# Kernel tuning notes

Hardware: AMD Instinct MI355X
Metric: run time of the kernel (lower is better)

## Reference

```python
import jax, jax.numpy as jnp
import numpy as np

N, H, F, E, K = 2048, 1024, 4096, 8, 2


def setup_inputs() -> dict:
    key = jax.random.key(0)
    ks = jax.random.split(key, 6)
    x = jax.random.normal(ks[0], (N, H), dtype=jnp.float32)
    mapping = jax.random.randint(ks[1], (N, K), 0, E)
    Wg = jax.random.normal(ks[2], (E, H), dtype=jnp.float32) * (1.0 / np.sqrt(H))
    W1 = jax.random.normal(ks[3], (E, H, F), dtype=jnp.float32) * (1.0 / np.sqrt(H))
    b1 = jnp.zeros((E, F), dtype=jnp.float32)
    W2 = jax.random.normal(ks[4], (E, F, H), dtype=jnp.float32) * (1.0 / np.sqrt(F))
    b2 = jnp.zeros((E, H), dtype=jnp.float32)
    return {"x": x, "mapping": mapping, "Wg": Wg, "W1": W1, "b1": b1, "W2": W2, "b2": b2}


def reference(x, mapping, Wg, W1, b1, W2, b2):
    # Gate logits: note original applies softmax over dim=0 (the token axis).
    logits = jax.nn.softmax(x @ Wg.T, axis=0)  # [N, E]

    # Per-expert MLP. Original sorts tokens by expert, runs per-expert GEMMs on
    # dynamic splits, then unsorts -- mathematically: y[i,k] = MLP_{mapping[i,k]}(x[i]).
    # JIT-friendly dense baseline: run every expert over all tokens, gather per token.
    def mlp(e):
        h = jax.nn.gelu(x @ W1[e] + b1[e])  # [N, F]
        return h @ W2[e] + b2[e]            # [N, H]

    y_all = jnp.stack([mlp(e) for e in range(E)])  # [E, N, H]

    # Gate weights gathered per (token, k), normalized over top-k.
    w = jnp.take_along_axis(logits, mapping, axis=1)  # [N, K]
    w = w / jnp.sum(w, axis=-1, keepdims=True)

    idx = jnp.arange(x.shape[0])
    out = jnp.zeros_like(x)
    for k in range(mapping.shape[1]):
        yk = y_all[mapping[:, k], idx]  # [N, H] gather per token's k-th expert
        out = out + yk * w[:, k:k + 1]
    return out
```

## Files before the change

### kernel.cpp

```cpp
#include <hip/hip_runtime.h>

#define N_TOK 2048
#define HD    1024
#define FD    4096
#define NE    8

typedef __attribute__((ext_vector_type(8))) short short8;
typedef __attribute__((ext_vector_type(4))) float floatx4;

__device__ __forceinline__ unsigned short f2bf(float f) {
  unsigned int u = __float_as_uint(f);
  u += 0x7fffu + ((u >> 16) & 1u);
  return (unsigned short)(u >> 16);
}

__device__ __forceinline__ void gl2lds16(const unsigned short* g, unsigned short* l) {
  __builtin_amdgcn_global_load_lds(
      (const __attribute__((address_space(1))) unsigned int*)g,
      (__attribute__((address_space(3))) unsigned int*)l, 16, 0, 0);
}

__device__ __forceinline__ float gelu_tanh(float x) {
  float t = 0.7978845608028654f * x * (1.0f + 0.044715f * x * x);
  return 0.5f * x * (1.0f + tanhf(t));
}

__device__ __forceinline__ int poff_of(const int* __restrict__ cnt, int e) {
  int o = 0;
  for (int i = 0; i < e; ++i) o += (cnt[i] + 127) & ~127;
  return o;
}

__global__ void k_gating(const float* __restrict__ x, const float* __restrict__ wg,
                         float* __restrict__ p) {
  int wave = threadIdx.x >> 6;
  int lane = threadIdx.x & 63;
  int n = blockIdx.x * 4 + wave;
  const float4* xr = (const float4*)(x + (size_t)n * HD);
  float4 xv[4];
  #pragma unroll
  for (int i = 0; i < 4; ++i) xv[i] = xr[lane + i * 64];
  for (int e = 0; e < NE; ++e) {
    const float4* wr = (const float4*)(wg + (size_t)e * HD);
    float s = 0.f;
    #pragma unroll
    for (int i = 0; i < 4; ++i) {
      float4 w4 = wr[lane + i * 64];
      s += xv[i].x * w4.x + xv[i].y * w4.y + xv[i].z * w4.z + xv[i].w * w4.w;
    }
    for (int o = 32; o > 0; o >>= 1) s += __shfl_xor(s, o, 64);
    if (lane == 0) p[e * N_TOK + n] = s;
  }
}

__global__ void k_softmax(float* __restrict__ p) {
  int e = blockIdx.x;
  float* col = p + e * N_TOK;
  __shared__ float red[256];
  int t = threadIdx.x;
  float m = -1e30f;
  for (int i = t; i < N_TOK; i += 256) m = fmaxf(m, col[i]);
  red[t] = m; __syncthreads();
  for (int s = 128; s > 0; s >>= 1) { if (t < s) red[t] = fmaxf(red[t], red[t + s]); __syncthreads(); }
  m = red[0]; __syncthreads();
  float sum = 0.f;
  for (int i = t; i < N_TOK; i += 256) { float v = expf(col[i] - m); col[i] = v; sum += v; }
  red[t] = sum; __syncthreads();
  for (int s = 128; s > 0; s >>= 1) { if (t < s) red[t] += red[t + s]; __syncthreads(); }
  float inv = 1.0f / red[0];
  for (int i = t; i < N_TOK; i += 256) col[i] *= inv;
}

__global__ void k_route(const int* __restrict__ mp, const float* __restrict__ p,
                        int* __restrict__ cnt, int* __restrict__ idxl,
                        int* __restrict__ tke, int* __restrict__ tks, float* __restrict__ tkw) {
  int n = blockIdx.x * 256 + threadIdx.x;
  if (n >= N_TOK) return;
  int m0 = mp[n * 2 + 0], m1 = mp[n * 2 + 1];
  if (m0 == m1) {
    int s = atomicAdd(&cnt[m0], 1);
    idxl[m0 * N_TOK + s] = n;
    tke[n * 2] = m0; tks[n * 2] = s; tkw[n * 2] = 1.0f;
    tke[n * 2 + 1] = m0; tks[n * 2 + 1] = s; tkw[n * 2 + 1] = 0.0f;
  } else {
    float p0 = p[m0 * N_TOK + n], p1 = p[m1 * N_TOK + n];
    float inv = 1.0f / (p0 + p1);
    int s0 = atomicAdd(&cnt[m0], 1);
    idxl[m0 * N_TOK + s0] = n;
    tke[n * 2] = m0; tks[n * 2] = s0; tkw[n * 2] = p0 * inv;
    int s1 = atomicAdd(&cnt[m1], 1);
    idxl[m1 * N_TOK + s1] = n;
    tke[n * 2 + 1] = m1; tks[n * 2 + 1] = s1; tkw[n * 2 + 1] = p1 * inv;
  }
}

__global__ void k_gather(const float* __restrict__ x, const int* __restrict__ cnt,
                         const int* __restrict__ idxl, unsigned short* __restrict__ xg) {
  int e = blockIdx.y;
  int r = blockIdx.x;
  int c = cnt[e];
  int pc = (c + 127) & ~127;
  if (r >= pc) return;
  unsigned short* dst = xg + ((size_t)poff_of(cnt, e) + r) * HD;
  int t = threadIdx.x;
  union { unsigned short us[8]; uint4 v; } o;
  if (r < c) {
    const float* src = x + (size_t)idxl[e * N_TOK + r] * HD;
    float4 f0 = ((const float4*)src)[t * 2];
    float4 f1 = ((const float4*)src)[t * 2 + 1];
    o.us[0] = f2bf(f0.x); o.us[1] = f2bf(f0.y); o.us[2] = f2bf(f0.z); o.us[3] = f2bf(f0.w);
    o.us[4] = f2bf(f1.x); o.us[5] = f2bf(f1.y); o.us[6] = f2bf(f1.z); o.us[7] = f2bf(f1.w);
  } else {
    o.v.x = 0u; o.v.y = 0u; o.v.z = 0u; o.v.w = 0u;
  }
  ((uint4*)dst)[t] = o.v;
}

__global__ __launch_bounds__(256) void k_transtile(const float* __restrict__ w1,
                                                   unsigned short* __restrict__ w1t,
                                                   const float* __restrict__ w2,
                                                   unsigned short* __restrict__ w2t) {
  __shared__ float tile[32][129];
  int l = blockIdx.x;
  const float* src; unsigned short* dst; int ncols; size_t tbase;
  int e, nt, kt;
  if (l < 8192) {
    e = l >> 10; nt = (l >> 5) & 31; kt = l & 31;
    src = w1 + (size_t)e * HD * FD; ncols = FD;
    dst = w1t; tbase = (((size_t)e * 32 + nt) * 32 + kt) * 4096;
  } else {
    int l2 = l - 8192;
    e = l2 >> 10; nt = (l2 >> 7) & 7; kt = l2 & 127;
    src = w2 + (size_t)e * FD * HD; ncols = HD;
    dst = w2t; tbase = (((size_t)e * 8 + nt) * 128 + kt) * 4096;
  }
  const int t = threadIdx.x;
  const int c4 = t & 31;
  const int rb = t >> 5;
  #pragma unroll
  for (int i = 0; i < 4; ++i) {
    int r = rb + 8 * i;
    float4 v = *(const float4*)(src + (size_t)(kt * 32 + r) * ncols + nt * 128 + c4 * 4);
    tile[r][c4 * 4 + 0] = v.x; tile[r][c4 * 4 + 1] = v.y;
    tile[r][c4 * 4 + 2] = v.z; tile[r][c4 * 4 + 3] = v.w;
  }
  __syncthreads();
  #pragma unroll
  for (int i = 0; i < 2; ++i) {
    int o = t * 2 + i;
    int n = o >> 2, kc = o & 3;
    union { unsigned short us[8]; uint4 v; } u;
    #pragma unroll
    for (int j = 0; j < 8; ++j) u.us[j] = f2bf(tile[kc * 8 + j][n]);
    *(uint4*)(dst + tbase + (size_t)o * 8) = u.v;
  }
}

__global__ __launch_bounds__(256) void k_gemm1(
    const unsigned short* __restrict__ xg, const unsigned short* __restrict__ w1t,
    const float* __restrict__ b1, const int* __restrict__ cnt,
    unsigned short* __restrict__ h) {
  const int l = blockIdx.x;
  const int r = l & 7;
  const int m = (l >> 3) & 31;
  const int q = l >> 8;
  const int e = q >> 2;
  const int n = ((q & 3) << 3) | r;

  const int c = cnt[e];
  const int mbase = m * 64;
  if (mbase >= c) return;
  const int nbase = n * 128;
  const int po = poff_of(cnt, e);
  const unsigned short* A = xg + ((size_t)po + mbase) * HD;
  const unsigned short* Bt = w1t + (((size_t)e * 32 + n) * 32) * 4096;

  __shared__ unsigned short As[64 * 32];
  __shared__ unsigned short Bs[128 * 32];

  const int tid = threadIdx.x;
  const int wave = tid >> 6, lane = tid & 63;
  const int quad = lane >> 4, lrow = lane & 15;
  const int wn = wave * 32;

  floatx4 acc[4][2];
  #pragma unroll
  for (int i = 0; i < 4; ++i)
    #pragma unroll
    for (int j = 0; j < 2; ++j) acc[i][j] = (floatx4){0.f, 0.f, 0.f, 0.f};

  const int rA = tid >> 2, kA = (tid & 3) * 8;

  for (int kt = 0; kt < HD / 32; ++kt) {
    __syncthreads();
    gl2lds16(A + kt * 32 + (size_t)rA * HD + kA, As + (size_t)wave * 512);
    const unsigned short* gb = Bt + (size_t)kt * 4096 + (size_t)tid * 8;
    gl2lds16(gb,        Bs + (size_t)wave * 512);
    gl2lds16(gb + 2048, Bs + 2048 + (size_t)wave * 512);
    __syncthreads();
    short8 aF[4], bF[2];
    #pragma unroll
    for (int i = 0; i < 4; ++i)
      aF[i] = *(const short8*)(As + (i * 16 + lrow) * 32 + quad * 8);
    #pragma unroll
    for (int j = 0; j < 2; ++j)
      bF[j] = *(const short8*)(Bs + (wn + j * 16 + lrow) * 32 + quad * 8);
    #pragma unroll
    for (int i = 0; i < 4; ++i)
      #pragma unroll
      for (int j = 0; j < 2; ++j)
        acc[i][j] = __builtin_amdgcn_mfma_f32_16x16x32_bf16(aF[i], bF[j], acc[i][j], 0, 0, 0);
  }

  const size_t hrow0 = (size_t)po + mbase;
  #pragma unroll
  for (int i = 0; i < 4; ++i) {
    #pragma unroll
    for (int rr = 0; rr < 4; ++rr) {
      int row = i * 16 + quad * 4 + rr;
      unsigned short* hr = h + (hrow0 + row) * FD + nbase;
      #pragma unroll
      for (int j = 0; j < 2; ++j) {
        int col = wn + j * 16 + lrow;
        float v = acc[i][j][rr] + b1[e * FD + nbase + col];
        hr[col] = f2bf(gelu_tanh(v));
      }
    }
  }
}

__global__ __launch_bounds__(256) void k_gemm2(
    const unsigned short* __restrict__ h, const unsigned short* __restrict__ w2t,
    const int* __restrict__ cnt, unsigned short* __restrict__ ya) {
  const int l = blockIdx.x;
  const int nt = l & 15;
  const int mt = l >> 4;
  const int mbase = mt * 64;
  const int nbase = nt * 64;

  int e = -1, po = 0, ce = 0;
  {
    int o = 0;
    #pragma unroll
    for (int i = 0; i < NE; ++i) {
      int ci = cnt[i];
      int pc = (ci + 127) & ~127;
      if (mbase >= o && mbase < o + pc) { e = i; po = o; ce = ci; }
      o += pc;
    }
  }
  if (e < 0) return;
  if (mbase - po >= ce) return;

  const unsigned short* A = h + (size_t)mbase * FD;
  const unsigned short* Bt = w2t + (((size_t)e * 8 + (nt >> 1)) * 128) * 4096
                                 + (size_t)(nt & 1) * 2048;

  __shared__ unsigned short As[2 * 64 * 32];
  __shared__ unsigned short Bs[2 * 64 * 32];

  const int tid = threadIdx.x;
  const int wave = tid >> 6, lane = tid & 63;
  const int quad = lane >> 4, lrow = lane & 15;
  const int wm = (wave >> 1) * 32, wn = (wave & 1) * 32;

  floatx4 acc[2][2];
  #pragma unroll
  for (int i = 0; i < 2; ++i)
    #pragma unroll
    for (int j = 0; j < 2; ++j) acc[i][j] = (floatx4){0.f, 0.f, 0.f, 0.f};

  const int r0 = tid >> 2, k0 = (tid & 3) * 8;

  for (int kt = 0; kt < FD / 64; ++kt) {
    __syncthreads();
    #pragma unroll
    for (int cc = 0; cc < 2; ++cc) {
      gl2lds16(A + (size_t)r0 * FD + kt * 64 + cc * 32 + k0,
               As + cc * 2048 + (size_t)wave * 512);
      gl2lds16(Bt + (size_t)(kt * 2 + cc) * 4096 + (size_t)tid * 8,
               Bs + cc * 2048 + (size_t)wave * 512);
    }
    __syncthreads();
    #pragma unroll
    for (int cc = 0; cc < 2; ++cc) {
      short8 aF[2], bF[2];
      #pragma unroll
      for (int i = 0; i < 2; ++i)
        aF[i] = *(const short8*)(As + cc * 2048 + (wm + i * 16 + lrow) * 32 + quad * 8);
      #pragma unroll
      for (int j = 0; j < 2; ++j)
        bF[j] = *(const short8*)(Bs + cc * 2048 + (wn + j * 16 + lrow) * 32 + quad * 8);
      #pragma unroll
      for (int i = 0; i < 2; ++i)
        #pragma unroll
        for (int j = 0; j < 2; ++j)
          acc[i][j] = __builtin_amdgcn_mfma_f32_16x16x32_bf16(aF[i], bF[j], acc[i][j], 0, 0, 0);
    }
  }

  #pragma unroll
  for (int i = 0; i < 2; ++i) {
    #pragma unroll
    for (int rr = 0; rr < 4; ++rr) {
      int row = mbase + wm + i * 16 + quad * 4 + rr;
      unsigned short* yr = ya + (size_t)row * HD + nbase;
      #pragma unroll
      for (int j = 0; j < 2; ++j) {
        int col = wn + j * 16 + lrow;
        yr[col] = f2bf(acc[i][j][rr]);
      }
    }
  }
}

__global__ __launch_bounds__(256) void k_combine(
    const unsigned short* __restrict__ ya, const float* __restrict__ b2,
    const int* __restrict__ cnt, const int* __restrict__ tke,
    const int* __restrict__ tks, const float* __restrict__ tkw,
    float* __restrict__ out) {
  int n = blockIdx.x;
  int e0 = tke[n * 2], e1 = tke[n * 2 + 1];
  int p0 = poff_of(cnt, e0) + tks[n * 2];
  int p1 = poff_of(cnt, e1) + tks[n * 2 + 1];
  float w0 = tkw[n * 2], w1 = tkw[n * 2 + 1];
  int c = threadIdx.x * 4;
  union { unsigned short us[4]; ushort2 u2[2]; unsigned long long ll; } y0, y1;
  y0.ll = *(const unsigned long long*)(ya + (size_t)p0 * HD + c);
  y1.ll = *(const unsigned long long*)(ya + (size_t)p1 * HD + c);
  float4 bb0 = *(const float4*)(b2 + (size_t)e0 * HD + c);
  float4 bb1 = *(const float4*)(b2 + (size_t)e1 * HD + c);
  float4 o;
  o.x = w0 * (__uint_as_float((unsigned)y0.us[0] << 16) + bb0.x) + w1 * (__uint_as_float((unsigned)y1.us[0] << 16) + bb1.x);
  o.y = w0 * (__uint_as_float((unsigned)y0.us[1] << 16) + bb0.y) + w1 * (__uint_as_float((unsigned)y1.us[1] << 16) + bb1.y);
  o.z = w0 * (__uint_as_float((unsigned)y0.us[2] << 16) + bb0.z) + w1 * (__uint_as_float((unsigned)y1.us[2] << 16) + bb1.z);
  o.w = w0 * (__uint_as_float((unsigned)y0.us[3] << 16) + bb0.w) + w1 * (__uint_as_float((unsigned)y1.us[3] << 16) + bb1.w);
  *(float4*)(out + (size_t)n * HD + c) = o;
}

extern "C" void kernel_launch(void* const* d_in, const int* in_sizes, int n_in,
                              void* d_out, int out_size, void* d_ws, size_t ws_size,
                              hipStream_t stream) {
  const float* x  = (const float*)d_in[0];
  const int*   mp = (const int*)d_in[1];
  const float* wg = (const float*)d_in[2];
  const float* w1 = (const float*)d_in[3];
  const float* b1 = (const float*)d_in[4];
  const float* w2 = (const float*)d_in[5];
  const float* b2 = (const float*)d_in[6];
  float* out = (float*)d_out;
  char* ws = (char*)d_ws;

  float* p    = (float*)(ws + 0);
  int*   cnt  = (int*)(ws + 65536);
  int*   idxl = (int*)(ws + 66048);
  int*   tke  = (int*)(ws + 131584);
  int*   tks  = (int*)(ws + 147968);
  float* tkw  = (float*)(ws + 164352);
  size_t off = 180736;
  unsigned short* w1t = (unsigned short*)(ws + off);  off += 67108864;
  unsigned short* w2t = (unsigned short*)(ws + off);  off += 67108864;
  unsigned short* xg  = (unsigned short*)(ws + off);  off += 10485760;
  unsigned short* h   = (unsigned short*)(ws + off);  off += 41943040;
  unsigned short* ya  = (unsigned short*)(ws + off);  off += 10485760;

  hipMemsetAsync(cnt, 0, 32, stream);

  k_gating<<<512, 256, 0, stream>>>(x, wg, p);
  k_softmax<<<NE, 256, 0, stream>>>(p);
  k_route<<<NE, 256, 0, stream>>>(mp, p, cnt, idxl, tke, tks, tkw);
  k_transtile<<<16384, 256, 0, stream>>>(w1, w1t, w2, w2t);
  k_gather<<<dim3(N_TOK, NE), 128, 0, stream>>>(x, cnt, idxl, xg);
  k_gemm1<<<8192, 256, 0, stream>>>(xg, w1t, b1, cnt, h);
  k_gemm2<<<80 * 16, 256, 0, stream>>>(h, w2t, cnt, ya);
  k_combine<<<N_TOK, 256, 0, stream>>>(ya, b2, cnt, tke, tks, tkw, out);
}
```

Measured before the change: 488.5 us.

## Fuse fp32 weight conversion and transpose into expert GEMM tile loads

Removes the separate weight transpose/bf16 conversion kernel and its 128MB workspace round trip. Each GEMM block now reads fp32 W1/W2 directly, converts to bf16 in registers, and writes into a XOR-swizzled LDS layout, with half the threads loading weights and half loading activations. Block indices are also remapped so blocks sharing a weight panel run on the same XCD, and gemm2 uses a per-expert grid instead of a scan. The trade-off is that weights are re-read and re-converted by every M tile. Weight loads also become plain fp32 global loads rather than async global-to-LDS copies, which may stall the inner loop.

```diff
diff --git a/kernel.cpp b/kernel.cpp
--- a/kernel.cpp
+++ b/kernel.cpp
@@ -116,64 +116,26 @@
   ((uint4*)dst)[t] = o.v;
 }
 
-__global__ __launch_bounds__(256) void k_transtile(const float* __restrict__ w1,
-                                                   unsigned short* __restrict__ w1t,
-                                                   const float* __restrict__ w2,
-                                                   unsigned short* __restrict__ w2t) {
-  __shared__ float tile[32][129];
-  int l = blockIdx.x;
-  const float* src; unsigned short* dst; int ncols; size_t tbase;
-  int e, nt, kt;
-  if (l < 8192) {
-    e = l >> 10; nt = (l >> 5) & 31; kt = l & 31;
-    src = w1 + (size_t)e * HD * FD; ncols = FD;
-    dst = w1t; tbase = (((size_t)e * 32 + nt) * 32 + kt) * 4096;
-  } else {
-    int l2 = l - 8192;
-    e = l2 >> 10; nt = (l2 >> 7) & 7; kt = l2 & 127;
-    src = w2 + (size_t)e * FD * HD; ncols = HD;
-    dst = w2t; tbase = (((size_t)e * 8 + nt) * 128 + kt) * 4096;
-  }
-  const int t = threadIdx.x;
-  const int c4 = t & 31;
-  const int rb = t >> 5;
-  #pragma unroll
-  for (int i = 0; i < 4; ++i) {
-    int r = rb + 8 * i;
-    float4 v = *(const float4*)(src + (size_t)(kt * 32 + r) * ncols + nt * 128 + c4 * 4);
-    tile[r][c4 * 4 + 0] = v.x; tile[r][c4 * 4 + 1] = v.y;
-    tile[r][c4 * 4 + 2] = v.z; tile[r][c4 * 4 + 3] = v.w;
-  }
-  __syncthreads();
-  #pragma unroll
-  for (int i = 0; i < 2; ++i) {
-    int o = t * 2 + i;
-    int n = o >> 2, kc = o & 3;
-    union { unsigned short us[8]; uint4 v; } u;
-    #pragma unroll
-    for (int j = 0; j < 8; ++j) u.us[j] = f2bf(tile[kc * 8 + j][n]);
-    *(uint4*)(dst + tbase + (size_t)o * 8) = u.v;
-  }
-}
-
 __global__ __launch_bounds__(256) void k_gemm1(
-    const unsigned short* __restrict__ xg, const unsigned short* __restrict__ w1t,
+    const unsigned short* __restrict__ xg, const float* __restrict__ w1,
     const float* __restrict__ b1, const int* __restrict__ cnt,
     unsigned short* __restrict__ h) {
-  const int l = blockIdx.x;
-  const int r = l & 7;
-  const int m = (l >> 3) & 31;
-  const int q = l >> 8;
-  const int e = q >> 2;
-  const int n = ((q & 3) << 3) | r;
+  const int b = blockIdx.x;
+  const int xcd = b & 7;
+  const int idx = b >> 3;
+  const int m = idx & 31;
+  const int panel = ((idx >> 5) << 3) + xcd;
+  const int e  = panel >> 5;
+  const int nt = panel & 31;
 
   const int c = cnt[e];
-  const int mbase = m * 64;
-  if (mbase >= c) return;
-  const int nbase = n * 128;
+  if (m * 64 >= c) return;
   const int po = poff_of(cnt, e);
-  const unsigned short* A = xg + ((size_t)po + mbase) * HD;
-  const unsigned short* Bt = w1t + (((size_t)e * 32 + n) * 32) * 4096;
+  const int nbase = nt * 128;
+  const size_t arow0 = (size_t)po + m * 64;
+
+  const unsigned short* A = xg + arow0 * HD;
+  const float* Bsrc = w1 + (size_t)e * HD * FD + nbase;
 
   __shared__ unsigned short As[64 * 32];
   __shared__ unsigned short Bs[128 * 32];
@@ -189,22 +151,44 @@
     #pragma unroll
     for (int j = 0; j < 2; ++j) acc[i][j] = (floatx4){0.f, 0.f, 0.f, 0.f};
 
-  const int rA = tid >> 2, kA = (tid & 3) * 8;
+  const int bg = tid & 31;
+  const int bq = (tid >> 5) & 3;
 
   for (int kt = 0; kt < HD / 32; ++kt) {
     __syncthreads();
-    gl2lds16(A + kt * 32 + (size_t)rA * HD + kA, As + (size_t)wave * 512);
-    const unsigned short* gb = Bt + (size_t)kt * 4096 + (size_t)tid * 8;
-    gl2lds16(gb,        Bs + (size_t)wave * 512);
-    gl2lds16(gb + 2048, Bs + 2048 + (size_t)wave * 512);
+    if (tid < 128) {
+      float4 f[8];
+      const float* src = Bsrc + (size_t)(kt * 32 + bq * 8) * FD + bg * 4;
+      #pragma unroll
+      for (int j = 0; j < 8; ++j)
+        f[j] = *(const float4*)(src + (size_t)j * FD);
+      #pragma unroll
+      for (int jn = 0; jn < 4; ++jn) {
+        int n = bg * 4 + jn;
+        union { unsigned short us[8]; uint4 v; } u;
+        #pragma unroll
+        for (int j = 0; j < 8; ++j) u.us[j] = f2bf(((const float*)&f[j])[jn]);
+        *(uint4*)(Bs + n * 32 + 8 * (bq ^ (bg & 3))) = u.v;
+      }
+    } else {
+      #pragma unroll
+      for (int i = 0; i < 2; ++i) {
+        int base = ((wave - 2) << 7) + (i << 6);
+        int ch = base + (tid & 63);
+        int row = ch >> 2, ko = (ch & 3) * 8;
+        gl2lds16(A + (size_t)row * HD + kt * 32 + ko, As + (size_t)base * 8);
+      }
+    }
     __syncthreads();
     short8 aF[4], bF[2];
     #pragma unroll
     for (int i = 0; i < 4; ++i)
       aF[i] = *(const short8*)(As + (i * 16 + lrow) * 32 + quad * 8);
     #pragma unroll
-    for (int j = 0; j < 2; ++j)
-      bF[j] = *(const short8*)(Bs + (wn + j * 16 + lrow) * 32 + quad * 8);
+    for (int j = 0; j < 2; ++j) {
+      int n = wn + j * 16 + lrow;
+      bF[j] = *(const short8*)(Bs + n * 32 + 8 * (quad ^ ((n >> 2) & 3)));
+    }
     #pragma unroll
     for (int i = 0; i < 4; ++i)
       #pragma unroll
@@ -212,13 +196,12 @@
         acc[i][j] = __builtin_amdgcn_mfma_f32_16x16x32_bf16(aF[i], bF[j], acc[i][j], 0, 0, 0);
   }
 
-  const size_t hrow0 = (size_t)po + mbase;
   #pragma unroll
   for (int i = 0; i < 4; ++i) {
     #pragma unroll
     for (int rr = 0; rr < 4; ++rr) {
       int row = i * 16 + quad * 4 + rr;
-      unsigned short* hr = h + (hrow0 + row) * FD + nbase;
+      unsigned short* hr = h + (arow0 + row) * FD + nbase;
       #pragma unroll
       for (int j = 0; j < 2; ++j) {
         int col = wn + j * 16 + lrow;
@@ -230,34 +213,27 @@
 }
 
 __global__ __launch_bounds__(256) void k_gemm2(
-    const unsigned short* __restrict__ h, const unsigned short* __restrict__ w2t,
+    const unsigned short* __restrict__ h, const float* __restrict__ w2,
     const int* __restrict__ cnt, unsigned short* __restrict__ ya) {
-  const int l = blockIdx.x;
-  const int nt = l & 15;
-  const int mt = l >> 4;
-  const int mbase = mt * 64;
+  const int b = blockIdx.x;
+  const int xcd = b & 7;
+  const int idx = b >> 3;
+  const int m = idx & 31;
+  const int panel = ((idx >> 5) << 3) + xcd;
+  const int e  = panel >> 4;
+  const int nt = panel & 15;
+
+  const int c = cnt[e];
+  if (m * 64 >= c) return;
+  const int po = poff_of(cnt, e);
   const int nbase = nt * 64;
-
-  int e = -1, po = 0, ce = 0;
-  {
-    int o = 0;
-    #pragma unroll
-    for (int i = 0; i < NE; ++i) {
-      int ci = cnt[i];
-      int pc = (ci + 127) & ~127;
-      if (mbase >= o && mbase < o + pc) { e = i; po = o; ce = ci; }
-      o += pc;
-    }
-  }
-  if (e < 0) return;
-  if (mbase - po >= ce) return;
-
-  const unsigned short* A = h + (size_t)mbase * FD;
-  const unsigned short* Bt = w2t + (((size_t)e * 8 + (nt >> 1)) * 128) * 4096
-                                 + (size_t)(nt & 1) * 2048;
-
-  __shared__ unsigned short As[2 * 64 * 32];
-  __shared__ unsigned short Bs[2 * 64 * 32];
+  const size_t arow0 = (size_t)po + m * 64;
+
+  const unsigned short* A = h + arow0 * FD;
+  const float* Bsrc = w2 + (size_t)e * FD * HD + nbase;
+
+  __shared__ unsigned short As[2][64 * 32];
+  __shared__ unsigned short Bs[2][64 * 32];
 
   const int tid = threadIdx.x;
   const int wave = tid >> 6, lane = tid & 63;
@@ -270,16 +246,35 @@
     #pragma unroll
     for (int j = 0; j < 2; ++j) acc[i][j] = (floatx4){0.f, 0.f, 0.f, 0.f};
 
-  const int r0 = tid >> 2, k0 = (tid & 3) * 8;
+  const int bg = tid & 15;
+  const int bq = (tid >> 4) & 7;
+  const int bh = bq >> 2, bq2 = bq & 3;
 
   for (int kt = 0; kt < FD / 64; ++kt) {
     __syncthreads();
-    #pragma unroll
-    for (int cc = 0; cc < 2; ++cc) {
-      gl2lds16(A + (size_t)r0 * FD + kt * 64 + cc * 32 + k0,
-               As + cc * 2048 + (size_t)wave * 512);
-      gl2lds16(Bt + (size_t)(kt * 2 + cc) * 4096 + (size_t)tid * 8,
-               Bs + cc * 2048 + (size_t)wave * 512);
+    if (tid < 128) {
+      float4 f[8];
+      const float* src = Bsrc + (size_t)(kt * 64 + bq * 8) * HD + bg * 4;
+      #pragma unroll
+      for (int j = 0; j < 8; ++j)
+        f[j] = *(const float4*)(src + (size_t)j * HD);
+      #pragma unroll
+      for (int jn = 0; jn < 4; ++jn) {
+        int n = bg * 4 + jn;
+        union { unsigned short us[8]; uint4 v; } u;
+        #pragma unroll
+        for (int j = 0; j < 8; ++j) u.us[j] = f2bf(((const float*)&f[j])[jn]);
+        *(uint4*)(Bs[bh] + n * 32 + 8 * (bq2 ^ (bg & 3))) = u.v;
+      }
+    } else {
+      #pragma unroll
+      for (int i = 0; i < 4; ++i) {
+        int half = i >> 1;
+        int base = ((i & 1) << 7) + ((wave & 1) << 6);
+        int ch = base + (tid & 63);
+        int row = ch >> 2, ko = (ch & 3) * 8 + half * 32;
+        gl2lds16(A + (size_t)row * FD + kt * 64 + ko, As[half] + (size_t)base * 8);
+      }
     }
     __syncthreads();
     #pragma unroll
@@ -287,10 +282,12 @@
       short8 aF[2], bF[2];
       #pragma unroll
       for (int i = 0; i < 2; ++i)
-        aF[i] = *(const short8*)(As + cc * 2048 + (wm + i * 16 + lrow) * 32 + quad * 8);
-      #pragma unroll
-      for (int j = 0; j < 2; ++j)
-        bF[j] = *(const short8*)(Bs + cc * 2048 + (wn + j * 16 + lrow) * 32 + quad * 8);
+        aF[i] = *(const short8*)(As[cc] + (wm + i * 16 + lrow) * 32 + quad * 8);
+      #pragma unroll
+      for (int j = 0; j < 2; ++j) {
+        int n = wn + j * 16 + lrow;
+        bF[j] = *(const short8*)(Bs[cc] + n * 32 + 8 * (quad ^ ((n >> 2) & 3)));
+      }
       #pragma unroll
       for (int i = 0; i < 2; ++i)
         #pragma unroll
@@ -303,8 +300,8 @@
   for (int i = 0; i < 2; ++i) {
     #pragma unroll
     for (int rr = 0; rr < 4; ++rr) {
-      int row = mbase + wm + i * 16 + quad * 4 + rr;
-      unsigned short* yr = ya + (size_t)row * HD + nbase;
+      size_t row = arow0 + wm + i * 16 + quad * 4 + rr;
+      unsigned short* yr = ya + row * HD + nbase;
       #pragma unroll
       for (int j = 0; j < 2; ++j) {
         int col = wn + j * 16 + lrow;
@@ -325,7 +322,7 @@
   int p1 = poff_of(cnt, e1) + tks[n * 2 + 1];
   float w0 = tkw[n * 2], w1 = tkw[n * 2 + 1];
   int c = threadIdx.x * 4;
-  union { unsigned short us[4]; ushort2 u2[2]; unsigned long long ll; } y0, y1;
+  union { unsigned short us[4]; unsigned long long ll; } y0, y1;
   y0.ll = *(const unsigned long long*)(ya + (size_t)p0 * HD + c);
   y1.ll = *(const unsigned long long*)(ya + (size_t)p1 * HD + c);
   float4 bb0 = *(const float4*)(b2 + (size_t)e0 * HD + c);
@@ -358,8 +355,6 @@
   int*   tks  = (int*)(ws + 147968);
   float* tkw  = (float*)(ws + 164352);
   size_t off = 180736;
-  unsigned short* w1t = (unsigned short*)(ws + off);  off += 67108864;
-  unsigned short* w2t = (unsigned short*)(ws + off);  off += 67108864;
   unsigned short* xg  = (unsigned short*)(ws + off);  off += 10485760;
   unsigned short* h   = (unsigned short*)(ws + off);  off += 41943040;
   unsigned short* ya  = (unsigned short*)(ws + off);  off += 10485760;
@@ -369,9 +364,8 @@
   k_gating<<<512, 256, 0, stream>>>(x, wg, p);
   k_softmax<<<NE, 256, 0, stream>>>(p);
   k_route<<<NE, 256, 0, stream>>>(mp, p, cnt, idxl, tke, tks, tkw);
-  k_transtile<<<16384, 256, 0, stream>>>(w1, w1t, w2, w2t);
   k_gather<<<dim3(N_TOK, NE), 128, 0, stream>>>(x, cnt, idxl, xg);
-  k_gemm1<<<8192, 256, 0, stream>>>(xg, w1t, b1, cnt, h);
-  k_gemm2<<<80 * 16, 256, 0, stream>>>(h, w2t, cnt, ya);
+  k_gemm1<<<8192, 256, 0, stream>>>(xg, w1, b1, cnt, h);
+  k_gemm2<<<4096, 256, 0, stream>>>(h, w2, cnt, ya);
   k_combine<<<N_TOK, 256, 0, stream>>>(ya, b2, cnt, tke, tks, tkw, out);
 }
```

Result: slower. 563.0 us (+15.2%).
